# Kernel optimization log

Measured on AMD Instinct MI355X. Metric: run time of the kernel, lower is better.

Reference implementation:

```python
import jax, jax.numpy as jnp
import numpy as np

E = 512
N = 8192
M = 4096
TEMPERATURE = 22.627416997969522  # sqrt(E)
EPS = 1e-6


def setup_inputs() -> dict:
    key = jax.random.key(0)
    k1, k2, k3, k4, k5 = jax.random.split(key, 5)
    s = 1.0 / np.sqrt(E)
    return {
        "v_code": jax.random.normal(k1, (N, E), dtype=jnp.float32),
        "obs_code": jax.random.normal(k2, (M, E), dtype=jnp.float32),
        "Wq": jax.random.normal(k3, (E, E), dtype=jnp.float32) * s,
        "Wk": jax.random.normal(k4, (E, E), dtype=jnp.float32) * s,
        "Wv": jax.random.normal(k5, (E, E), dtype=jnp.float32) * s,
        "gamma": jnp.ones((E,), dtype=jnp.float32),
        "beta": jnp.zeros((E,), dtype=jnp.float32),
    }


def _layer_norm(x, gamma, beta):
    mu = jnp.mean(x, axis=-1, keepdims=True)
    var = jnp.mean(jnp.square(x - mu), axis=-1, keepdims=True)
    return (x - mu) * jax.lax.rsqrt(var + EPS) * gamma + beta


def reference(v_code, obs_code, Wq, Wk, Wv, gamma, beta):
    # torch Linear: y = x @ W.T (no bias)
    v_value = v_code @ Wv.T          # [N, E]
    obs_value = obs_code @ Wv.T      # [M, E]
    v_query = v_code @ Wq.T          # [N, E]
    v_key = v_code @ Wk.T            # [N, E]
    obs_key = obs_code @ Wk.T        # [M, E]

    obs_attention = v_query @ obs_key.T                 # [N, M] cross attention
    self_attention = jnp.sum(v_query * v_key, axis=-1)  # [N] diagonal self score

    whole = jnp.concatenate([self_attention[:, None], obs_attention], axis=-1)  # [N, M+1]
    w = jax.nn.softmax(whole / TEMPERATURE, axis=-1)

    # weighted sum over concat([v_value_i, obs_value...]) without materializing
    # the [N, M+1, E] repeat tensor: same math as the torch code.
    v_code_new = w[:, :1] * v_value + w[:, 1:] @ obs_value  # [N, E]

    return _layer_norm(v_code_new + v_code, gamma, beta)
```

## Files before the change

kernel.cpp:

```cpp
#include <hip/hip_runtime.h>
#include <hip/hip_bf16.h>

typedef unsigned short u16;
typedef __bf16 bf16x8 __attribute__((ext_vector_type(8)));
typedef float f32x4 __attribute__((ext_vector_type(4)));

#define N_ROWS 8192
#define M_ROWS 4096
#define E_DIM  512
#define KSPLIT 4
#define INV_T  0.04419417382415922f

__device__ __forceinline__ u16 f2bf(float f) {
    unsigned u = __float_as_uint(f);
    u += 0x7FFF + ((u >> 16) & 1);
    return (u16)(u >> 16);
}
__device__ __forceinline__ float bf2f(u16 u) {
    return __uint_as_float(((unsigned)u) << 16);
}

#define GLD16(gp, lp) \
    __builtin_amdgcn_global_load_lds((const __attribute__((address_space(1))) void*)(gp), \
                                     (__attribute__((address_space(3))) void*)(lp), 16, 0, 0)

__global__ __launch_bounds__(256)
void cast_bf(const float* __restrict__ in, u16* __restrict__ out, int n4) {
    int i = blockIdx.x * 256 + threadIdx.x;
    if (i < n4) {
        float4 f = reinterpret_cast<const float4*>(in)[i];
        ushort4 o;
        o.x = f2bf(f.x); o.y = f2bf(f.y); o.z = f2bf(f.z); o.w = f2bf(f.w);
        reinterpret_cast<ushort4*>(out)[i] = o;
    }
}

__global__ __launch_bounds__(256)
void transpose_bf(const u16* __restrict__ in, u16* __restrict__ out, int R, int C) {
    __shared__ u16 t[64][72];
    const int r0 = blockIdx.y * 64, c0 = blockIdx.x * 64;
    const int tid = threadIdx.x;
    const int lr = tid >> 2, lc = (tid & 3) * 16;
    const u16* src = in + (size_t)(r0 + lr) * C + c0 + lc;
    *reinterpret_cast<uint4*>(&t[lr][lc])     = *reinterpret_cast<const uint4*>(src);
    *reinterpret_cast<uint4*>(&t[lr][lc + 8]) = *reinterpret_cast<const uint4*>(src + 8);
    __syncthreads();
    u16 tmp[16];
#pragma unroll
    for (int j = 0; j < 16; ++j) tmp[j] = t[lc + j][lr];
    u16* dst = out + (size_t)(c0 + lr) * R + r0 + lc;
    *reinterpret_cast<uint4*>(dst)     = *reinterpret_cast<uint4*>(&tmp[0]);
    *reinterpret_cast<uint4*>(dst + 8) = *reinterpret_cast<uint4*>(&tmp[8]);
}

__device__ __forceinline__
void gemm_wide_body(const u16* __restrict__ A, int lda,
                    const u16* __restrict__ B, int ldb,
                    void* __restrict__ C, int ldc, int K,
                    int row0, int col0, int mode,
                    float* __restrict__ psum ) {
    __shared__ u16 sA[2][128 * 32];
    __shared__ u16 sB[2][256 * 32];

    const int tid  = threadIdx.x;
    const int wave = tid >> 6, lane = tid & 63;
    const int quad = lane >> 4, m16 = lane & 15;
    const int wr = (wave & 1) * 64;
    const int wc = (wave >> 1) * 128;

    const int srow  = lane >> 2;
    const int skoff = (lane & 3) * 8;
    const u16* ag0 = A + (size_t)(row0 + wave * 16 + srow) * lda + skoff;
    const u16* ag1 = ag0 + (size_t)64 * lda;
    const u16* bg0 = B + (size_t)(col0 + wave * 16 + srow) * ldb + skoff;
    const u16* bg1 = bg0 + (size_t)64 * ldb;
    const u16* bg2 = bg0 + (size_t)128 * ldb;
    const u16* bg3 = bg0 + (size_t)192 * ldb;
    const int loa0 = (wave * 16) * 32;
    const int loa1 = (wave * 16 + 64) * 32;
    const int lob0 = (wave * 16) * 32;
    const int lob1 = (wave * 16 + 64) * 32;
    const int lob2 = (wave * 16 + 128) * 32;
    const int lob3 = (wave * 16 + 192) * 32;

    f32x4 acc[4][8];
#pragma unroll
    for (int i = 0; i < 4; ++i)
#pragma unroll
        for (int j = 0; j < 8; ++j) acc[i][j] = (f32x4){0.f, 0.f, 0.f, 0.f};

    GLD16(ag0, &sA[0][loa0]); GLD16(ag1, &sA[0][loa1]);
    GLD16(bg0, &sB[0][lob0]); GLD16(bg1, &sB[0][lob1]);
    GLD16(bg2, &sB[0][lob2]); GLD16(bg3, &sB[0][lob3]);

    int kb = 0;
    for (int k0 = 0; k0 < K; k0 += 32, kb ^= 1) {
        __syncthreads();
        const int kn = (k0 + 32 < K) ? (k0 + 32) : 0;
        GLD16(ag0 + kn, &sA[kb ^ 1][loa0]); GLD16(ag1 + kn, &sA[kb ^ 1][loa1]);
        GLD16(bg0 + kn, &sB[kb ^ 1][lob0]); GLD16(bg1 + kn, &sB[kb ^ 1][lob1]);
        GLD16(bg2 + kn, &sB[kb ^ 1][lob2]); GLD16(bg3 + kn, &sB[kb ^ 1][lob3]);

        bf16x8 a[4], b[8];
#pragma unroll
        for (int i = 0; i < 4; ++i)
            a[i] = *reinterpret_cast<const bf16x8*>(&sA[kb][(wr + i * 16 + m16) * 32 + quad * 8]);
#pragma unroll
        for (int j = 0; j < 8; ++j)
            b[j] = *reinterpret_cast<const bf16x8*>(&sB[kb][(wc + j * 16 + m16) * 32 + quad * 8]);
#pragma unroll
        for (int i = 0; i < 4; ++i)
#pragma unroll
            for (int j = 0; j < 8; ++j)
                acc[i][j] = __builtin_amdgcn_mfma_f32_16x16x32_bf16(a[i], b[j], acc[i][j], 0, 0, 0);
    }

    if (mode == 2) {
        float* pcol = psum + (size_t)(wave >> 1) * N_ROWS;
#pragma unroll
        for (int i = 0; i < 4; ++i) {
            const int rbase = row0 + wr + i * 16 + quad * 4;
            float rs[4] = {0.f, 0.f, 0.f, 0.f};
#pragma unroll
            for (int j = 0; j < 8; ++j) {
                const int c = col0 + wc + j * 16 + m16;
#pragma unroll
                for (int r = 0; r < 4; ++r) {
                    const float v = __expf(acc[i][j][r] * INV_T);
                    rs[r] += v;
                    reinterpret_cast<u16*>(C)[(size_t)(rbase + r) * ldc + c] = f2bf(v);
                }
            }
#pragma unroll
            for (int r = 0; r < 4; ++r) {
                float s = rs[r];
                s += __shfl_down(s, 8, 16);
                s += __shfl_down(s, 4, 16);
                s += __shfl_down(s, 2, 16);
                s += __shfl_down(s, 1, 16);
                if (m16 == 0) pcol[rbase + r] = s;
            }
        }
    } else {
#pragma unroll
        for (int i = 0; i < 4; ++i) {
            const int rbase = row0 + wr + i * 16 + quad * 4;
#pragma unroll
            for (int j = 0; j < 8; ++j) {
                const int c = col0 + wc + j * 16 + m16;
#pragma unroll
                for (int r = 0; r < 4; ++r) {
                    const float v = acc[i][j][r];
                    const int rr = rbase + r;
                    if (mode == 0) {
                        reinterpret_cast<float*>(C)[(size_t)rr * ldc + c] = v;
                    } else {
                        reinterpret_cast<u16*>(C)[(size_t)rr * ldc + c] = f2bf(v);
                    }
                }
            }
        }
    }
}

struct ProjArgs {
    const u16* A[3];
    const u16* B[3];
    void*      C[3];
    int        rows[3];
    int        mode[3];
    int        ldc[3];
};

__global__ __launch_bounds__(256, 2)
void proj_gemm(ProjArgs p) {
    const int z = blockIdx.z;
    const int row0 = blockIdx.y * 128;
    if (row0 >= p.rows[z]) return;
    gemm_wide_body(p.A[z], E_DIM, p.B[z], E_DIM, p.C[z], p.ldc[z], E_DIM,
                   row0, blockIdx.x * 256, p.mode[z], nullptr);
}

__global__ __launch_bounds__(256, 2)
void gemm_main(const u16* __restrict__ A, int lda,
               const u16* __restrict__ B, int ldb,
               void* __restrict__ C, int ldc, int Kslice,
               long long cstride_bytes, int mode, float* __restrict__ psum) {
    const int z = blockIdx.z;
    const u16* Az = A + (long long)z * Kslice;
    const u16* Bz = B + (long long)z * Kslice;
    void* Cz = (char*)C + (long long)z * cstride_bytes;
    float* ps = psum ? psum + (size_t)(blockIdx.x * 2) * N_ROWS : nullptr;
    gemm_wide_body(Az, lda, Bz, ldb, Cz, ldc, Kslice,
                   blockIdx.y * 128, blockIdx.x * 256, mode, ps);
}

__global__ __launch_bounds__(256)
void self_dot(const u16* __restrict__ q, const u16* __restrict__ k,
              float* __restrict__ selfS) {
    const int wave = threadIdx.x >> 6, lane = threadIdx.x & 63;
    const int row = blockIdx.x * 4 + wave;
    const uint4 qa = *reinterpret_cast<const uint4*>(q + (size_t)row * E_DIM + lane * 8);
    const uint4 ka = *reinterpret_cast<const uint4*>(k + (size_t)row * E_DIM + lane * 8);
    unsigned qu[4] = {qa.x, qa.y, qa.z, qa.w};
    unsigned ku[4] = {ka.x, ka.y, ka.z, ka.w};
    float s = 0.f;
#pragma unroll
    for (int i = 0; i < 4; ++i) {
        s += bf2f((u16)(qu[i] & 0xFFFF)) * bf2f((u16)(ku[i] & 0xFFFF));
        s += bf2f((u16)(qu[i] >> 16))    * bf2f((u16)(ku[i] >> 16));
    }
#pragma unroll
    for (int off = 32; off; off >>= 1) s += __shfl_down(s, off);
    if (lane == 0) selfS[row] = s;
}

__global__ __launch_bounds__(256)
void sum_combine(const float* __restrict__ psum, const float* __restrict__ selfS,
                 float* __restrict__ p0_out, float* __restrict__ invl_out) {
    const int n = blockIdx.x * 256 + threadIdx.x;
    float l = 0.f;
#pragma unroll
    for (int j = 0; j < 32; ++j) l += psum[(size_t)j * N_ROWS + n];
    const float p0 = expf(selfS[n] * INV_T);
    l += p0;
    p0_out[n] = p0;
    invl_out[n] = 1.f / l;
}

__global__ __launch_bounds__(256)
void final_ln(const u16* __restrict__ O ,
              const u16* __restrict__ vval ,
              const float* __restrict__ p0v, const float* __restrict__ invl,
              const float* __restrict__ vcode,
              const float* __restrict__ gamma, const float* __restrict__ beta,
              float* __restrict__ out) {
    __shared__ float lds[8];
    const int n = blockIdx.x, t = threadIdx.x;
    const int lane = t & 63, wave = t >> 6;
    const size_t base = (size_t)n * E_DIM;
    const size_t NE = (size_t)N_ROWS * E_DIM;
    const float a = p0v[n], il = invl[n];

    float o0 = 0.f, o1 = 0.f;
#pragma unroll
    for (int z = 0; z < KSPLIT; ++z) {
        o0 += bf2f(O[z * NE + base + t]);
        o1 += bf2f(O[z * NE + base + t + 256]);
    }
    float x0 = fmaf(a, bf2f(vval[base + t]),       o0) * il + vcode[base + t];
    float x1 = fmaf(a, bf2f(vval[base + t + 256]), o1) * il + vcode[base + t + 256];

    float s = x0 + x1;
#pragma unroll
    for (int off = 32; off; off >>= 1) s += __shfl_down(s, off);
    if (lane == 0) lds[wave] = s;
    __syncthreads();
    const float mu = (lds[0] + lds[1] + lds[2] + lds[3]) * (1.0f / E_DIM);
    __syncthreads();

    const float d0 = x0 - mu, d1 = x1 - mu;
    float vs = d0 * d0 + d1 * d1;
#pragma unroll
    for (int off = 32; off; off >>= 1) vs += __shfl_down(vs, off);
    if (lane == 0) lds[wave] = vs;
    __syncthreads();
    const float var = (lds[0] + lds[1] + lds[2] + lds[3]) * (1.0f / E_DIM);
    const float rs = rsqrtf(var + 1e-6f);

    out[base + t]       = d0 * rs * gamma[t]       + beta[t];
    out[base + t + 256] = d1 * rs * gamma[t + 256] + beta[t + 256];
}

#define OFF_VCODEBF 0ull
#define OFF_OBSBF   8388608ull
#define OFF_WQ      12582912ull
#define OFF_WK      13107200ull
#define OFF_WV      13631488ull
#define OFF_WQT     14155776ull
#define OFF_WKT     14680064ull
#define OFF_WQKT    15204352ull
#define OFF_TBF     15728640ull
#define OFF_OBSV    24117248ull
#define OFF_OBSVT   28311552ull
#define OFF_VVAL    32505856ull
#define OFF_S       49283072ull
#define OFF_O       116391936ull
#define OFF_P0      149946368ull
#define OFF_SELF    149979136ull
#define OFF_INVL    150011904ull
#define OFF_PSUM    150044672ull

extern "C" void kernel_launch(void* const* d_in, const int* in_sizes, int n_in,
                              void* d_out, int out_size, void* d_ws, size_t ws_size,
                              hipStream_t stream) {
    const float* v_code   = (const float*)d_in[0];
    const float* obs_code = (const float*)d_in[1];
    const float* Wq       = (const float*)d_in[2];
    const float* Wk       = (const float*)d_in[3];
    const float* Wv       = (const float*)d_in[4];
    const float* gamma    = (const float*)d_in[5];
    const float* beta     = (const float*)d_in[6];
    float* out = (float*)d_out;
    char* ws = (char*)d_ws;

    u16* vcode_bf = (u16*)(ws + OFF_VCODEBF);
    u16* obs_bf   = (u16*)(ws + OFF_OBSBF);
    u16* wq_bf    = (u16*)(ws + OFF_WQ);
    u16* wk_bf    = (u16*)(ws + OFF_WK);
    u16* wv_bf    = (u16*)(ws + OFF_WV);
    u16* wqT      = (u16*)(ws + OFF_WQT);
    u16* wkT      = (u16*)(ws + OFF_WKT);
    u16* wqkT     = (u16*)(ws + OFF_WQKT);
    u16* t_bf     = (u16*)(ws + OFF_TBF);
    u16* obsv_bf  = (u16*)(ws + OFF_OBSV);
    u16* obsvT_bf = (u16*)(ws + OFF_OBSVT);
    u16* vval     = (u16*)(ws + OFF_VVAL);
    u16* S        = (u16*)(ws + OFF_S);
    u16* O        = (u16*)(ws + OFF_O);
    float* p0v    = (float*)(ws + OFF_P0);
    float* selfS  = (float*)(ws + OFF_SELF);
    float* invl   = (float*)(ws + OFF_INVL);
    float* psum   = (float*)(ws + OFF_PSUM);

    cast_bf<<<N_ROWS * E_DIM / 4 / 256, 256, 0, stream>>>(v_code, vcode_bf, N_ROWS * E_DIM / 4);
    cast_bf<<<M_ROWS * E_DIM / 4 / 256, 256, 0, stream>>>(obs_code, obs_bf, M_ROWS * E_DIM / 4);
    cast_bf<<<E_DIM * E_DIM / 4 / 256, 256, 0, stream>>>(Wq, wq_bf, E_DIM * E_DIM / 4);
    cast_bf<<<E_DIM * E_DIM / 4 / 256, 256, 0, stream>>>(Wk, wk_bf, E_DIM * E_DIM / 4);
    cast_bf<<<E_DIM * E_DIM / 4 / 256, 256, 0, stream>>>(Wv, wv_bf, E_DIM * E_DIM / 4);

    transpose_bf<<<dim3(8, 8), 256, 0, stream>>>(wq_bf, wqT, E_DIM, E_DIM);
    transpose_bf<<<dim3(8, 8), 256, 0, stream>>>(wk_bf, wkT, E_DIM, E_DIM);

    gemm_main<<<dim3(E_DIM / 256, E_DIM / 128, 1), 256, 0, stream>>>(
        wkT, E_DIM, wqT, E_DIM, wqkT, E_DIM, E_DIM, 0, 1, nullptr);

    ProjArgs p;
    p.A[0] = vcode_bf; p.B[0] = wv_bf; p.C[0] = vval;    p.rows[0] = N_ROWS; p.mode[0] = 1; p.ldc[0] = E_DIM;
    p.A[1] = obs_bf;   p.B[1] = wv_bf; p.C[1] = obsv_bf; p.rows[1] = M_ROWS; p.mode[1] = 1; p.ldc[1] = E_DIM;
    p.A[2] = vcode_bf; p.B[2] = wqkT;  p.C[2] = t_bf;    p.rows[2] = N_ROWS; p.mode[2] = 1; p.ldc[2] = E_DIM;
    proj_gemm<<<dim3(E_DIM / 256, N_ROWS / 128, 3), 256, 0, stream>>>(p);

    transpose_bf<<<dim3(E_DIM / 64, M_ROWS / 64), 256, 0, stream>>>(obsv_bf, obsvT_bf, M_ROWS, E_DIM);

    self_dot<<<N_ROWS / 4, 256, 0, stream>>>(t_bf, vcode_bf, selfS);

    gemm_main<<<dim3(M_ROWS / 256, N_ROWS / 128, 1), 256, 0, stream>>>(
        t_bf, E_DIM, obs_bf, E_DIM, S, M_ROWS, E_DIM, 0, 2, psum);

    sum_combine<<<N_ROWS / 256, 256, 0, stream>>>(psum, selfS, p0v, invl);

    gemm_main<<<dim3(E_DIM / 256, N_ROWS / 128, KSPLIT), 256, 0, stream>>>(
        S, M_ROWS, obsvT_bf, M_ROWS, O, E_DIM, M_ROWS / KSPLIT,
        (long long)N_ROWS * E_DIM * 2, 1, nullptr);

    final_ln<<<N_ROWS, 256, 0, stream>>>(O, vval, p0v, invl, v_code, gamma, beta, out);
}
```

Before: 266.4 us.

## Fuse score GEMM, exp, and PV GEMM into a flash-style kernel

Result: slower. 327.2 us (+22.8%).

```diff
diff --git a/kernel.cpp b/kernel.cpp
--- a/kernel.cpp
+++ b/kernel.cpp
@@ -57,8 +57,7 @@
 void gemm_wide_body(const u16* __restrict__ A, int lda,
                     const u16* __restrict__ B, int ldb,
                     void* __restrict__ C, int ldc, int K,
-                    int row0, int col0, int mode,
-                    float* __restrict__ psum ) {
+                    int row0, int col0, int mode) {
     __shared__ u16 sA[2][128 * 32];
     __shared__ u16 sB[2][256 * 32];
 
@@ -115,48 +114,20 @@
                 acc[i][j] = __builtin_amdgcn_mfma_f32_16x16x32_bf16(a[i], b[j], acc[i][j], 0, 0, 0);
     }
 
-    if (mode == 2) {
-        float* pcol = psum + (size_t)(wave >> 1) * N_ROWS;
-#pragma unroll
-        for (int i = 0; i < 4; ++i) {
-            const int rbase = row0 + wr + i * 16 + quad * 4;
-            float rs[4] = {0.f, 0.f, 0.f, 0.f};
-#pragma unroll
-            for (int j = 0; j < 8; ++j) {
-                const int c = col0 + wc + j * 16 + m16;
-#pragma unroll
-                for (int r = 0; r < 4; ++r) {
-                    const float v = __expf(acc[i][j][r] * INV_T);
-                    rs[r] += v;
-                    reinterpret_cast<u16*>(C)[(size_t)(rbase + r) * ldc + c] = f2bf(v);
-                }
-            }
+#pragma unroll
+    for (int i = 0; i < 4; ++i) {
+        const int rbase = row0 + wr + i * 16 + quad * 4;
+#pragma unroll
+        for (int j = 0; j < 8; ++j) {
+            const int c = col0 + wc + j * 16 + m16;
 #pragma unroll
             for (int r = 0; r < 4; ++r) {
-                float s = rs[r];
-                s += __shfl_down(s, 8, 16);
-                s += __shfl_down(s, 4, 16);
-                s += __shfl_down(s, 2, 16);
-                s += __shfl_down(s, 1, 16);
-                if (m16 == 0) pcol[rbase + r] = s;
-            }
-        }
-    } else {
-#pragma unroll
-        for (int i = 0; i < 4; ++i) {
-            const int rbase = row0 + wr + i * 16 + quad * 4;
-#pragma unroll
-            for (int j = 0; j < 8; ++j) {
-                const int c = col0 + wc + j * 16 + m16;
-#pragma unroll
-                for (int r = 0; r < 4; ++r) {
-                    const float v = acc[i][j][r];
-                    const int rr = rbase + r;
-                    if (mode == 0) {
-                        reinterpret_cast<float*>(C)[(size_t)rr * ldc + c] = v;
-                    } else {
-                        reinterpret_cast<u16*>(C)[(size_t)rr * ldc + c] = f2bf(v);
-                    }
+                const float v = acc[i][j][r];
+                const int rr = rbase + r;
+                if (mode == 0) {
+                    reinterpret_cast<float*>(C)[(size_t)rr * ldc + c] = v;
+                } else {
+                    reinterpret_cast<u16*>(C)[(size_t)rr * ldc + c] = f2bf(v);
                 }
             }
         }
@@ -178,21 +149,156 @@
     const int row0 = blockIdx.y * 128;
     if (row0 >= p.rows[z]) return;
     gemm_wide_body(p.A[z], E_DIM, p.B[z], E_DIM, p.C[z], p.ldc[z], E_DIM,
-                   row0, blockIdx.x * 256, p.mode[z], nullptr);
+                   row0, blockIdx.x * 256, p.mode[z]);
 }
 
 __global__ __launch_bounds__(256, 2)
 void gemm_main(const u16* __restrict__ A, int lda,
                const u16* __restrict__ B, int ldb,
-               void* __restrict__ C, int ldc, int Kslice,
-               long long cstride_bytes, int mode, float* __restrict__ psum) {
-    const int z = blockIdx.z;
-    const u16* Az = A + (long long)z * Kslice;
-    const u16* Bz = B + (long long)z * Kslice;
-    void* Cz = (char*)C + (long long)z * cstride_bytes;
-    float* ps = psum ? psum + (size_t)(blockIdx.x * 2) * N_ROWS : nullptr;
-    gemm_wide_body(Az, lda, Bz, ldb, Cz, ldc, Kslice,
-                   blockIdx.y * 128, blockIdx.x * 256, mode, ps);
+               void* __restrict__ C, int ldc, int K, int mode) {
+    gemm_wide_body(A, lda, B, ldb, C, ldc, K,
+                   blockIdx.y * 128, blockIdx.x * 256, mode);
+}
+
+__global__ __launch_bounds__(512, 1)
+void flash_pv(const u16* __restrict__ T, const u16* __restrict__ OBS,
+              const u16* __restrict__ VT, u16* __restrict__ O,
+              float* __restrict__ psum) {
+    __shared__ u16 sT[2][64 * 32];
+    __shared__ u16 sOV[2][256 * 32];
+    __shared__ u16 sP[64 * 264];
+
+    const int b = blockIdx.x;
+    const int zj = (b & 7) >> 1;
+    const int q0 = ((b >> 3) * 2 + (b & 1)) * 64;
+    const int tid = threadIdx.x;
+    const int wave = tid >> 6, lane = tid & 63;
+    const int quad = lane >> 4, m16 = lane & 15;
+    const int srow = lane >> 2, skoff = (lane & 3) * 8;
+    const int tl = wave * 512 + lane * 8;
+
+    const u16* tg  = T + (size_t)(q0 + wave * 16 + srow) * E_DIM + skoff;
+    const u16* vt0 = VT + (size_t)(wave * 16 + srow) * M_ROWS + skoff;
+
+    f32x4 accO[4][4];
+#pragma unroll
+    for (int i = 0; i < 4; ++i)
+#pragma unroll
+        for (int j = 0; j < 4; ++j) accO[i][j] = (f32x4){0.f, 0.f, 0.f, 0.f};
+    float racc[4][4];
+#pragma unroll
+    for (int i = 0; i < 4; ++i)
+#pragma unroll
+        for (int r = 0; r < 4; ++r) racc[i][r] = 0.f;
+
+    for (int c = 0; c < 4; ++c) {
+        const int jb = zj * 1024 + c * 256;
+        const u16* og = OBS + (size_t)(jb + wave * 16 + srow) * E_DIM + skoff;
+
+        f32x4 accS[4][2];
+#pragma unroll
+        for (int i = 0; i < 4; ++i) {
+            accS[i][0] = (f32x4){0.f, 0.f, 0.f, 0.f};
+            accS[i][1] = (f32x4){0.f, 0.f, 0.f, 0.f};
+        }
+
+        __syncthreads();
+        if (wave < 4) GLD16(tg, &sT[0][tl]);
+        GLD16(og,               &sOV[0][tl]);
+        GLD16(og + 128 * E_DIM, &sOV[0][tl + 4096]);
+
+        int kb = 0;
+        for (int k0 = 0; k0 < E_DIM; k0 += 32, kb ^= 1) {
+            __syncthreads();
+            if (k0 + 32 < E_DIM) {
+                if (wave < 4) GLD16(tg + k0 + 32, &sT[kb ^ 1][tl]);
+                GLD16(og + k0 + 32,               &sOV[kb ^ 1][tl]);
+                GLD16(og + 128 * E_DIM + k0 + 32, &sOV[kb ^ 1][tl + 4096]);
+            }
+            bf16x8 a[4], bb[2];
+#pragma unroll
+            for (int i = 0; i < 4; ++i)
+                a[i] = *reinterpret_cast<const bf16x8*>(&sT[kb][(i * 16 + m16) * 32 + quad * 8]);
+#pragma unroll
+            for (int j = 0; j < 2; ++j)
+                bb[j] = *reinterpret_cast<const bf16x8*>(
+                    &sOV[kb][(wave * 32 + j * 16 + m16) * 32 + quad * 8]);
+#pragma unroll
+            for (int i = 0; i < 4; ++i)
+#pragma unroll
+                for (int j = 0; j < 2; ++j)
+                    accS[i][j] = __builtin_amdgcn_mfma_f32_16x16x32_bf16(a[i], bb[j], accS[i][j], 0, 0, 0);
+        }
+
+#pragma unroll
+        for (int i = 0; i < 4; ++i) {
+            float rs[4] = {0.f, 0.f, 0.f, 0.f};
+#pragma unroll
+            for (int j = 0; j < 2; ++j) {
+                const int col = wave * 32 + j * 16 + m16;
+#pragma unroll
+                for (int r = 0; r < 4; ++r) {
+                    const float v = __expf(accS[i][j][r] * INV_T);
+                    rs[r] += v;
+                    sP[(i * 16 + quad * 4 + r) * 264 + col] = f2bf(v);
+                }
+            }
+#pragma unroll
+            for (int r = 0; r < 4; ++r) {
+                float s = rs[r];
+                s += __shfl_down(s, 8, 16);
+                s += __shfl_down(s, 4, 16);
+                s += __shfl_down(s, 2, 16);
+                s += __shfl_down(s, 1, 16);
+                racc[i][r] += s;
+            }
+        }
+
+        u16* sV = &sOV[0][0];
+        for (int jj = 0; jj < 256; jj += 32) {
+            __syncthreads();
+            const u16* v0 = vt0 + jb + jj;
+            GLD16(v0,                &sV[tl]);
+            GLD16(v0 + 128 * M_ROWS, &sV[tl + 4096]);
+            GLD16(v0 + 256 * M_ROWS, &sV[tl + 8192]);
+            GLD16(v0 + 384 * M_ROWS, &sV[tl + 12288]);
+            __syncthreads();
+            bf16x8 a2[4], b2[4];
+#pragma unroll
+            for (int i = 0; i < 4; ++i)
+                a2[i] = *reinterpret_cast<const bf16x8*>(&sP[(i * 16 + m16) * 264 + jj + quad * 8]);
+#pragma unroll
+            for (int j = 0; j < 4; ++j)
+                b2[j] = *reinterpret_cast<const bf16x8*>(
+                    &sV[(wave * 64 + j * 16 + m16) * 32 + quad * 8]);
+#pragma unroll
+            for (int i = 0; i < 4; ++i)
+#pragma unroll
+                for (int j = 0; j < 4; ++j)
+                    accO[i][j] = __builtin_amdgcn_mfma_f32_16x16x32_bf16(a2[i], b2[j], accO[i][j], 0, 0, 0);
+        }
+    }
+
+    u16* Oz = O + (size_t)zj * N_ROWS * E_DIM;
+#pragma unroll
+    for (int i = 0; i < 4; ++i) {
+        const int rbase = q0 + i * 16 + quad * 4;
+#pragma unroll
+        for (int j = 0; j < 4; ++j) {
+            const int cc = wave * 64 + j * 16 + m16;
+#pragma unroll
+            for (int r = 0; r < 4; ++r)
+                Oz[(size_t)(rbase + r) * E_DIM + cc] = f2bf(accO[i][j][r]);
+        }
+    }
+    if (m16 == 0) {
+        float* ps = psum + (size_t)(zj * 8 + wave) * N_ROWS;
+#pragma unroll
+        for (int i = 0; i < 4; ++i)
+#pragma unroll
+            for (int r = 0; r < 4; ++r)
+                ps[q0 + i * 16 + quad * 4 + r] = racc[i][r];
+    }
 }
 
 __global__ __launch_bounds__(256)
@@ -229,8 +335,7 @@
 }
 
 __global__ __launch_bounds__(256)
-void final_ln(const u16* __restrict__ O ,
-              const u16* __restrict__ vval ,
+void final_ln(const u16* __restrict__ O, const u16* __restrict__ vval,
               const float* __restrict__ p0v, const float* __restrict__ invl,
               const float* __restrict__ vcode,
               const float* __restrict__ gamma, const float* __restrict__ beta,
@@ -284,12 +389,11 @@
 #define OFF_OBSV    24117248ull
 #define OFF_OBSVT   28311552ull
 #define OFF_VVAL    32505856ull
-#define OFF_S       49283072ull
-#define OFF_O       116391936ull
-#define OFF_P0      149946368ull
-#define OFF_SELF    149979136ull
-#define OFF_INVL    150011904ull
-#define OFF_PSUM    150044672ull
+#define OFF_O       40894464ull
+#define OFF_P0      74448896ull
+#define OFF_SELF    74481664ull
+#define OFF_INVL    74514432ull
+#define OFF_PSUM    74547200ull
 
 extern "C" void kernel_launch(void* const* d_in, const int* in_sizes, int n_in,
                               void* d_out, int out_size, void* d_ws, size_t ws_size,
@@ -316,7 +420,6 @@
     u16* obsv_bf  = (u16*)(ws + OFF_OBSV);
     u16* obsvT_bf = (u16*)(ws + OFF_OBSVT);
     u16* vval     = (u16*)(ws + OFF_VVAL);
-    u16* S        = (u16*)(ws + OFF_S);
     u16* O        = (u16*)(ws + OFF_O);
     float* p0v    = (float*)(ws + OFF_P0);
     float* selfS  = (float*)(ws + OFF_SELF);
@@ -333,7 +436,7 @@
     transpose_bf<<<dim3(8, 8), 256, 0, stream>>>(wk_bf, wkT, E_DIM, E_DIM);
 
     gemm_main<<<dim3(E_DIM / 256, E_DIM / 128, 1), 256, 0, stream>>>(
-        wkT, E_DIM, wqT, E_DIM, wqkT, E_DIM, E_DIM, 0, 1, nullptr);
+        wkT, E_DIM, wqT, E_DIM, wqkT, E_DIM, E_DIM, 1);
 
     ProjArgs p;
     p.A[0] = vcode_bf; p.B[0] = wv_bf; p.C[0] = vval;    p.rows[0] = N_ROWS; p.mode[0] = 1; p.ldc[0] = E_DIM;
@@ -345,14 +448,9 @@
 
     self_dot<<<N_ROWS / 4, 256, 0, stream>>>(t_bf, vcode_bf, selfS);
 
-    gemm_main<<<dim3(M_ROWS / 256, N_ROWS / 128, 1), 256, 0, stream>>>(
-        t_bf, E_DIM, obs_bf, E_DIM, S, M_ROWS, E_DIM, 0, 2, psum);
+    flash_pv<<<512, 512, 0, stream>>>(t_bf, obs_bf, obsvT_bf, O, psum);
 
     sum_combine<<<N_ROWS / 256, 256, 0, stream>>>(psum, selfS, p0v, invl);
 
-    gemm_main<<<dim3(E_DIM / 256, N_ROWS / 128, KSPLIT), 256, 0, stream>>>(
-        S, M_ROWS, obsvT_bf, M_ROWS, O, E_DIM, M_ROWS / KSPLIT,
-        (long long)N_ROWS * E_DIM * 2, 1, nullptr);
-
     final_ln<<<N_ROWS, 256, 0, stream>>>(O, vval, p0v, invl, v_code, gamma, beta, out);
 }
```

## Store softmax probabilities and transposed values in FP8 and run PV GEMM in FP8

Applied to the files above, without the earlier changes.

After: 255.7 us. 1.04x faster.

```diff
diff --git a/kernel.cpp b/kernel.cpp
--- a/kernel.cpp
+++ b/kernel.cpp
@@ -2,6 +2,7 @@
 #include <hip/hip_bf16.h>
 
 typedef unsigned short u16;
+typedef unsigned char u8;
 typedef __bf16 bf16x8 __attribute__((ext_vector_type(8)));
 typedef float f32x4 __attribute__((ext_vector_type(4)));
 
@@ -18,6 +19,10 @@
 }
 __device__ __forceinline__ float bf2f(u16 u) {
     return __uint_as_float(((unsigned)u) << 16);
+}
+__device__ __forceinline__ u8 f2fp8(float f) {
+    int p = __builtin_amdgcn_cvt_pk_fp8_f32(f, f, 0, false);
+    return (u8)(p & 0xFF);
 }
 
 #define GLD16(gp, lp) \
@@ -35,8 +40,41 @@
     }
 }
 
-__global__ __launch_bounds__(256)
-void transpose_bf(const u16* __restrict__ in, u16* __restrict__ out, int R, int C) {
+struct WCastArgs { const float* src[3]; u16* dst[3]; };
+__global__ __launch_bounds__(256)
+void cast_w3(WCastArgs a) {
+    const int z = blockIdx.z;
+    const int i = blockIdx.x * 256 + threadIdx.x;
+    float4 f = reinterpret_cast<const float4*>(a.src[z])[i];
+    ushort4 o;
+    o.x = f2bf(f.x); o.y = f2bf(f.y); o.z = f2bf(f.z); o.w = f2bf(f.w);
+    reinterpret_cast<ushort4*>(a.dst[z])[i] = o;
+}
+
+__global__ __launch_bounds__(256)
+void transpose_w2(const u16* __restrict__ in0, u16* __restrict__ out0,
+                  const u16* __restrict__ in1, u16* __restrict__ out1) {
+    __shared__ u16 t[64][72];
+    const u16* in = blockIdx.z ? in1 : in0;
+    u16* out      = blockIdx.z ? out1 : out0;
+    const int R = E_DIM, C = E_DIM;
+    const int r0 = blockIdx.y * 64, c0 = blockIdx.x * 64;
+    const int tid = threadIdx.x;
+    const int lr = tid >> 2, lc = (tid & 3) * 16;
+    const u16* src = in + (size_t)(r0 + lr) * C + c0 + lc;
+    *reinterpret_cast<uint4*>(&t[lr][lc])     = *reinterpret_cast<const uint4*>(src);
+    *reinterpret_cast<uint4*>(&t[lr][lc + 8]) = *reinterpret_cast<const uint4*>(src + 8);
+    __syncthreads();
+    u16 tmp[16];
+#pragma unroll
+    for (int j = 0; j < 16; ++j) tmp[j] = t[lc + j][lr];
+    u16* dst = out + (size_t)(c0 + lr) * R + r0 + lc;
+    *reinterpret_cast<uint4*>(dst)     = *reinterpret_cast<uint4*>(&tmp[0]);
+    *reinterpret_cast<uint4*>(dst + 8) = *reinterpret_cast<uint4*>(&tmp[8]);
+}
+
+__global__ __launch_bounds__(256)
+void transpose_to_fp8(const u16* __restrict__ in, u8* __restrict__ out, int R, int C) {
     __shared__ u16 t[64][72];
     const int r0 = blockIdx.y * 64, c0 = blockIdx.x * 64;
     const int tid = threadIdx.x;
@@ -45,20 +83,26 @@
     *reinterpret_cast<uint4*>(&t[lr][lc])     = *reinterpret_cast<const uint4*>(src);
     *reinterpret_cast<uint4*>(&t[lr][lc + 8]) = *reinterpret_cast<const uint4*>(src + 8);
     __syncthreads();
-    u16 tmp[16];
-#pragma unroll
-    for (int j = 0; j < 16; ++j) tmp[j] = t[lc + j][lr];
-    u16* dst = out + (size_t)(c0 + lr) * R + r0 + lc;
-    *reinterpret_cast<uint4*>(dst)     = *reinterpret_cast<uint4*>(&tmp[0]);
-    *reinterpret_cast<uint4*>(dst + 8) = *reinterpret_cast<uint4*>(&tmp[8]);
+    unsigned w[4];
+#pragma unroll
+    for (int g = 0; g < 4; ++g) {
+        float f0 = bf2f(t[lc + 4 * g + 0][lr]);
+        float f1 = bf2f(t[lc + 4 * g + 1][lr]);
+        float f2 = bf2f(t[lc + 4 * g + 2][lr]);
+        float f3 = bf2f(t[lc + 4 * g + 3][lr]);
+        int p01 = __builtin_amdgcn_cvt_pk_fp8_f32(f0, f1, 0, false);
+        int p23 = __builtin_amdgcn_cvt_pk_fp8_f32(f2, f3, 0, false);
+        w[g] = (unsigned)(p01 & 0xFFFF) | ((unsigned)p23 << 16);
+    }
+    u8* dst = out + (size_t)(c0 + lr) * R + r0 + lc;
+    *reinterpret_cast<uint4*>(dst) = (uint4){w[0], w[1], w[2], w[3]};
 }
 
 __device__ __forceinline__
 void gemm_wide_body(const u16* __restrict__ A, int lda,
                     const u16* __restrict__ B, int ldb,
                     void* __restrict__ C, int ldc, int K,
-                    int row0, int col0, int mode,
-                    float* __restrict__ psum ) {
+                    int row0, int col0, int mode, float* __restrict__ psum) {
     __shared__ u16 sA[2][128 * 32];
     __shared__ u16 sB[2][256 * 32];
 
@@ -128,7 +172,7 @@
                 for (int r = 0; r < 4; ++r) {
                     const float v = __expf(acc[i][j][r] * INV_T);
                     rs[r] += v;
-                    reinterpret_cast<u16*>(C)[(size_t)(rbase + r) * ldc + c] = f2bf(v);
+                    reinterpret_cast<u8*>(C)[(size_t)(rbase + r) * ldc + c] = f2fp8(v);
                 }
             }
 #pragma unroll
@@ -149,15 +193,8 @@
             for (int j = 0; j < 8; ++j) {
                 const int c = col0 + wc + j * 16 + m16;
 #pragma unroll
-                for (int r = 0; r < 4; ++r) {
-                    const float v = acc[i][j][r];
-                    const int rr = rbase + r;
-                    if (mode == 0) {
-                        reinterpret_cast<float*>(C)[(size_t)rr * ldc + c] = v;
-                    } else {
-                        reinterpret_cast<u16*>(C)[(size_t)rr * ldc + c] = f2bf(v);
-                    }
-                }
+                for (int r = 0; r < 4; ++r)
+                    reinterpret_cast<u16*>(C)[(size_t)(rbase + r) * ldc + c] = f2bf(acc[i][j][r]);
             }
         }
     }
@@ -168,7 +205,6 @@
     const u16* B[3];
     void*      C[3];
     int        rows[3];
-    int        mode[3];
     int        ldc[3];
 };
 
@@ -178,21 +214,81 @@
     const int row0 = blockIdx.y * 128;
     if (row0 >= p.rows[z]) return;
     gemm_wide_body(p.A[z], E_DIM, p.B[z], E_DIM, p.C[z], p.ldc[z], E_DIM,
-                   row0, blockIdx.x * 256, p.mode[z], nullptr);
+                   row0, blockIdx.x * 256, 1, nullptr);
 }
 
 __global__ __launch_bounds__(256, 2)
 void gemm_main(const u16* __restrict__ A, int lda,
                const u16* __restrict__ B, int ldb,
-               void* __restrict__ C, int ldc, int Kslice,
-               long long cstride_bytes, int mode, float* __restrict__ psum) {
+               void* __restrict__ C, int ldc, int K, int mode,
+               float* __restrict__ psum) {
+    float* ps = psum ? psum + (size_t)(blockIdx.x * 2) * N_ROWS : nullptr;
+    gemm_wide_body(A, lda, B, ldb, C, ldc, K,
+                   blockIdx.y * 128, blockIdx.x * 256, mode, ps);
+}
+
+__global__ __launch_bounds__(256, 2)
+void pv_fp8(const u8* __restrict__ P, const u8* __restrict__ VT,
+            u16* __restrict__ O, int Kslice) {
+    __shared__ u8 sA[2][128 * 32];
+    __shared__ u8 sB[2][256 * 32];
+
     const int z = blockIdx.z;
-    const u16* Az = A + (long long)z * Kslice;
-    const u16* Bz = B + (long long)z * Kslice;
-    void* Cz = (char*)C + (long long)z * cstride_bytes;
-    float* ps = psum ? psum + (size_t)(blockIdx.x * 2) * N_ROWS : nullptr;
-    gemm_wide_body(Az, lda, Bz, ldb, Cz, ldc, Kslice,
-                   blockIdx.y * 128, blockIdx.x * 256, mode, ps);
+    const int row0 = blockIdx.y * 128, col0 = blockIdx.x * 256;
+    const int tid = threadIdx.x;
+    const int wave = tid >> 6, lane = tid & 63;
+    const int quad = lane >> 4, m16 = lane & 15;
+    const int wr = (wave & 1) * 64, wc = (wave >> 1) * 128;
+    const int trow = tid >> 1, toff = (tid & 1) * 16;
+
+    const u8* ag  = P  + (size_t)(row0 + trow) * M_ROWS + z * Kslice + toff;
+    const u8* bg0 = VT + (size_t)(col0 + trow) * M_ROWS + z * Kslice + toff;
+    const u8* bg1 = bg0 + (size_t)128 * M_ROWS;
+
+    f32x4 acc[4][8];
+#pragma unroll
+    for (int i = 0; i < 4; ++i)
+#pragma unroll
+        for (int j = 0; j < 8; ++j) acc[i][j] = (f32x4){0.f, 0.f, 0.f, 0.f};
+
+    GLD16(ag,  &sA[0][tid * 16]);
+    GLD16(bg0, &sB[0][tid * 16]);
+    GLD16(bg1, &sB[0][4096 + tid * 16]);
+
+    int kb = 0;
+    for (int k0 = 0; k0 < Kslice; k0 += 32, kb ^= 1) {
+        __syncthreads();
+        const int kn = (k0 + 32 < Kslice) ? (k0 + 32) : 0;
+        GLD16(ag + kn,  &sA[kb ^ 1][tid * 16]);
+        GLD16(bg0 + kn, &sB[kb ^ 1][tid * 16]);
+        GLD16(bg1 + kn, &sB[kb ^ 1][4096 + tid * 16]);
+
+        long a[4], b[8];
+#pragma unroll
+        for (int i = 0; i < 4; ++i)
+            a[i] = *reinterpret_cast<const long*>(&sA[kb][(wr + i * 16 + m16) * 32 + quad * 8]);
+#pragma unroll
+        for (int j = 0; j < 8; ++j)
+            b[j] = *reinterpret_cast<const long*>(&sB[kb][(wc + j * 16 + m16) * 32 + quad * 8]);
+#pragma unroll
+        for (int i = 0; i < 4; ++i)
+#pragma unroll
+            for (int j = 0; j < 8; ++j)
+                acc[i][j] = __builtin_amdgcn_mfma_f32_16x16x32_fp8_fp8(a[i], b[j], acc[i][j], 0, 0, 0);
+    }
+
+    u16* Oz = O + (size_t)z * N_ROWS * E_DIM;
+#pragma unroll
+    for (int i = 0; i < 4; ++i) {
+        const int rbase = row0 + wr + i * 16 + quad * 4;
+#pragma unroll
+        for (int j = 0; j < 8; ++j) {
+            const int c = col0 + wc + j * 16 + m16;
+#pragma unroll
+            for (int r = 0; r < 4; ++r)
+                Oz[(size_t)(rbase + r) * E_DIM + c] = f2bf(acc[i][j][r]);
+        }
+    }
 }
 
 __global__ __launch_bounds__(256)
@@ -229,8 +325,7 @@
 }
 
 __global__ __launch_bounds__(256)
-void final_ln(const u16* __restrict__ O ,
-              const u16* __restrict__ vval ,
+void final_ln(const u16* __restrict__ O, const u16* __restrict__ vval,
               const float* __restrict__ p0v, const float* __restrict__ invl,
               const float* __restrict__ vcode,
               const float* __restrict__ gamma, const float* __restrict__ beta,
@@ -282,14 +377,14 @@
 #define OFF_WQKT    15204352ull
 #define OFF_TBF     15728640ull
 #define OFF_OBSV    24117248ull
-#define OFF_OBSVT   28311552ull
-#define OFF_VVAL    32505856ull
-#define OFF_S       49283072ull
-#define OFF_O       116391936ull
-#define OFF_P0      149946368ull
-#define OFF_SELF    149979136ull
-#define OFF_INVL    150011904ull
-#define OFF_PSUM    150044672ull
+#define OFF_OBSVT8  28311552ull
+#define OFF_VVAL    30408704ull
+#define OFF_S8      38797312ull
+#define OFF_O       72351744ull
+#define OFF_P0      105906176ull
+#define OFF_SELF    105938944ull
+#define OFF_INVL    105971712ull
+#define OFF_PSUM    106004480ull
 
 extern "C" void kernel_launch(void* const* d_in, const int* in_sizes, int n_in,
                               void* d_out, int out_size, void* d_ws, size_t ws_size,
@@ -314,9 +409,9 @@
     u16* wqkT     = (u16*)(ws + OFF_WQKT);
     u16* t_bf     = (u16*)(ws + OFF_TBF);
     u16* obsv_bf  = (u16*)(ws + OFF_OBSV);
-    u16* obsvT_bf = (u16*)(ws + OFF_OBSVT);
+    u8*  obsvT8   = (u8*)(ws + OFF_OBSVT8);
     u16* vval     = (u16*)(ws + OFF_VVAL);
-    u16* S        = (u16*)(ws + OFF_S);
+    u8*  S8       = (u8*)(ws + OFF_S8);
     u16* O        = (u16*)(ws + OFF_O);
     float* p0v    = (float*)(ws + OFF_P0);
     float* selfS  = (float*)(ws + OFF_SELF);
@@ -325,34 +420,35 @@
 
     cast_bf<<<N_ROWS * E_DIM / 4 / 256, 256, 0, stream>>>(v_code, vcode_bf, N_ROWS * E_DIM / 4);
     cast_bf<<<M_ROWS * E_DIM / 4 / 256, 256, 0, stream>>>(obs_code, obs_bf, M_ROWS * E_DIM / 4);
-    cast_bf<<<E_DIM * E_DIM / 4 / 256, 256, 0, stream>>>(Wq, wq_bf, E_DIM * E_DIM / 4);
-    cast_bf<<<E_DIM * E_DIM / 4 / 256, 256, 0, stream>>>(Wk, wk_bf, E_DIM * E_DIM / 4);
-    cast_bf<<<E_DIM * E_DIM / 4 / 256, 256, 0, stream>>>(Wv, wv_bf, E_DIM * E_DIM / 4);
-
-    transpose_bf<<<dim3(8, 8), 256, 0, stream>>>(wq_bf, wqT, E_DIM, E_DIM);
-    transpose_bf<<<dim3(8, 8), 256, 0, stream>>>(wk_bf, wkT, E_DIM, E_DIM);
+    WCastArgs wc;
+    wc.src[0] = Wq; wc.dst[0] = wq_bf;
+    wc.src[1] = Wk; wc.dst[1] = wk_bf;
+    wc.src[2] = Wv; wc.dst[2] = wv_bf;
+    cast_w3<<<dim3(E_DIM * E_DIM / 4 / 256, 1, 3), 256, 0, stream>>>(wc);
+
+    transpose_w2<<<dim3(8, 8, 2), 256, 0, stream>>>(wq_bf, wqT, wk_bf, wkT);
 
     gemm_main<<<dim3(E_DIM / 256, E_DIM / 128, 1), 256, 0, stream>>>(
-        wkT, E_DIM, wqT, E_DIM, wqkT, E_DIM, E_DIM, 0, 1, nullptr);
+        wkT, E_DIM, wqT, E_DIM, wqkT, E_DIM, E_DIM, 1, nullptr);
 
     ProjArgs p;
-    p.A[0] = vcode_bf; p.B[0] = wv_bf; p.C[0] = vval;    p.rows[0] = N_ROWS; p.mode[0] = 1; p.ldc[0] = E_DIM;
-    p.A[1] = obs_bf;   p.B[1] = wv_bf; p.C[1] = obsv_bf; p.rows[1] = M_ROWS; p.mode[1] = 1; p.ldc[1] = E_DIM;
-    p.A[2] = vcode_bf; p.B[2] = wqkT;  p.C[2] = t_bf;    p.rows[2] = N_ROWS; p.mode[2] = 1; p.ldc[2] = E_DIM;
+    p.A[0] = vcode_bf; p.B[0] = wv_bf; p.C[0] = vval;    p.rows[0] = N_ROWS; p.ldc[0] = E_DIM;
+    p.A[1] = obs_bf;   p.B[1] = wv_bf; p.C[1] = obsv_bf; p.rows[1] = M_ROWS; p.ldc[1] = E_DIM;
+    p.A[2] = vcode_bf; p.B[2] = wqkT;  p.C[2] = t_bf;    p.rows[2] = N_ROWS; p.ldc[2] = E_DIM;
     proj_gemm<<<dim3(E_DIM / 256, N_ROWS / 128, 3), 256, 0, stream>>>(p);
 
-    transpose_bf<<<dim3(E_DIM / 64, M_ROWS / 64), 256, 0, stream>>>(obsv_bf, obsvT_bf, M_ROWS, E_DIM);
+    transpose_to_fp8<<<dim3(E_DIM / 64, M_ROWS / 64), 256, 0, stream>>>(
+        obsv_bf, obsvT8, M_ROWS, E_DIM);
 
     self_dot<<<N_ROWS / 4, 256, 0, stream>>>(t_bf, vcode_bf, selfS);
 
     gemm_main<<<dim3(M_ROWS / 256, N_ROWS / 128, 1), 256, 0, stream>>>(
-        t_bf, E_DIM, obs_bf, E_DIM, S, M_ROWS, E_DIM, 0, 2, psum);
+        t_bf, E_DIM, obs_bf, E_DIM, S8, M_ROWS, E_DIM, 2, psum);
 
     sum_combine<<<N_ROWS / 256, 256, 0, stream>>>(psum, selfS, p0v, invl);
 
-    gemm_main<<<dim3(E_DIM / 256, N_ROWS / 128, KSPLIT), 256, 0, stream>>>(
-        S, M_ROWS, obsvT_bf, M_ROWS, O, E_DIM, M_ROWS / KSPLIT,
-        (long long)N_ROWS * E_DIM * 2, 1, nullptr);
+    pv_fp8<<<dim3(E_DIM / 256, N_ROWS / 128, KSPLIT), 256, 0, stream>>>(
+        S8, obsvT8, O, M_ROWS / KSPLIT);
 
     final_ln<<<N_ROWS, 256, 0, stream>>>(O, vval, p0v, invl, v_code, gamma, beta, out);
 }
```
